# Performance work log

Measured on AMD Instinct MI355X. Metric: run time of the kernel, lower is better.

## Reference

```python
import jax, jax.numpy as jnp
import numpy as np
import math

N, E, D, H = 50000, 1600000, 128, 8
DH = D // H  # per-head dim
EPS = 1e-5   # batchnorm eps


def _attn(q_in, k_in, v_in, Wq, Wk, Wv, src, dst):
    # GAT-style edge attention: score = exp(clip(<K[src],Q[dst]>/sqrt(DH), -5, 5))
    Q = (q_in @ Wq.T).reshape(-1, H, DH)
    K = (k_in @ Wk.T).reshape(-1, H, DH)
    V = (v_in @ Wv.T).reshape(-1, H, DH)
    score = jnp.exp(jnp.clip((K[src] * Q[dst]).sum(-1) / math.sqrt(DH), -5.0, 5.0))  # [E,H]
    wV = jax.ops.segment_sum(V[src] * score[:, :, None], dst, num_segments=N)  # [N,H,DH]
    z = jax.ops.segment_sum(score, dst, num_segments=N)                         # [N,H]
    return (wV / z[:, :, None]).reshape(-1, D)


def _bn(x, gamma, beta):
    # BatchNorm1d in training mode: biased batch stats over nodes
    m = x.mean(0)
    v = x.var(0)
    return (x - m) / jnp.sqrt(v + EPS) * gamma + beta


def setup_inputs() -> dict:
    key = jax.random.key(0)
    ks = iter(jax.random.split(key, 48))

    def w(shape, scale=None):
        s = scale if scale is not None else 1.0 / math.sqrt(shape[-1])
        return jax.random.normal(next(ks), shape, jnp.float32) * s

    inp = dict(
        h=w((N, D), 1.0),
        sv=w((N, D), 1.0),
        src=jax.random.randint(next(ks), (E,), 0, N, jnp.int32),
        dst=jax.random.randint(next(ks), (E,), 0, N, jnp.int32),
    )
    for nm in ["Wq_sv", "Wk_sv", "Wv_sv", "Wq_cv", "Wk_cv", "Wv_cv",
               "Wq_sh", "Wk_sh", "Wv_sh"]:
        inp[nm] = w((D, D))
    inp.update(
        Wo=w((D, 2 * D)), bo=jnp.zeros((D,), jnp.float32),
        Wo_h=w((D, 2 * D)), bo_h=jnp.zeros((D,), jnp.float32),
        W1=w((2 * D, D)), b1=jnp.zeros((2 * D,), jnp.float32),
        W2=w((D, 2 * D)), b2=jnp.zeros((D,), jnp.float32),
        W1h=w((2 * D, D)), b1h=jnp.zeros((2 * D,), jnp.float32),
        W2h=w((D, 2 * D)), b2h=jnp.zeros((D,), jnp.float32),
        Wg1=w((D, D)), bg1=jnp.zeros((D,), jnp.float32),
        Wg2=w((D, D)), bg2=jnp.zeros((D,), jnp.float32),
        gbn1=jnp.ones((D,), jnp.float32), bbn1=jnp.zeros((D,), jnp.float32),
        gbn2=jnp.ones((D,), jnp.float32), bbn2=jnp.zeros((D,), jnp.float32),
        gbn1h=jnp.ones((D,), jnp.float32), bbn1h=jnp.zeros((D,), jnp.float32),
        gbn2h=jnp.ones((D,), jnp.float32), bbn2h=jnp.zeros((D,), jnp.float32),
    )
    return inp


def reference(h, sv, src, dst,
              Wq_sv, Wk_sv, Wv_sv, Wq_cv, Wk_cv, Wv_cv, Wq_sh, Wk_sh, Wv_sh,
              Wo, bo, Wo_h, bo_h,
              W1, b1, W2, b2, W1h, b1h, W2h, b2h,
              Wg1, bg1, Wg2, bg2,
              gbn1, bbn1, gbn2, bbn2, gbn1h, bbn1h, gbn2h, bbn2h):
    h_in1, sv_in1 = h, sv
    # --- h branch ---
    a_self = _attn(h, h, h, Wq_sv, Wk_sv, Wv_sv, src, dst)
    a_cross = _attn(h, sv, sv, Wq_cv, Wk_cv, Wv_cv, src, dst)
    hO = jnp.concatenate([a_self, a_cross], -1) @ Wo.T + bo
    h1 = _bn(h_in1 + hO, gbn1, bbn1)
    ffn = jax.nn.relu(h1 @ W1.T + b1) @ W2.T + b2
    h_out = _bn(h1 + ffn, gbn2, bbn2)
    # --- state-vector branch ---
    a_self_h = _attn(sv, sv, sv, Wq_sh, Wk_sh, Wv_sh, src, dst)
    # faithful to source: cross_attention_v weights reused here
    a_cross_h = _attn(sv, h_in1, h_in1, Wq_cv, Wk_cv, Wv_cv, src, dst)
    svO = jnp.concatenate([a_self_h, a_cross_h], -1) @ Wo_h.T + bo_h
    g1 = jax.nn.sigmoid(h_in1 @ Wg1.T + bg1)
    sv1 = _bn((1.0 - g1) * sv_in1 + g1 * svO, gbn1h, bbn1h)
    ffn_h = jax.nn.relu(sv1 @ W1h.T + b1h) @ W2h.T + b2h
    g2 = jax.nn.sigmoid(h_in1 @ Wg2.T + bg2)
    sv_out = _bn((1.0 - g2) * sv1 + g2 * ffn_h, gbn2h, bbn2h)
    return (h_out, sv_out)
```

## Files before the change

### kernel.cpp

```cpp
#include <hip/hip_runtime.h>

typedef _Float16 f16x8 __attribute__((ext_vector_type(8)));
typedef _Float16 f16x2 __attribute__((ext_vector_type(2)));
typedef __fp16 fp16x2_raw __attribute__((ext_vector_type(2)));
typedef float f32x4 __attribute__((ext_vector_type(4)));
typedef float f32x2 __attribute__((ext_vector_type(2)));
typedef unsigned int uint32;
typedef unsigned short ushort16;
typedef unsigned char uchar;

#define EPS_BN 1e-5f

__device__ __forceinline__ uint32 pk16(float a, float b){
  fp16x2_raw h = __builtin_amdgcn_cvt_pkrtz(a, b);
  return *(uint32*)&h;
}
__device__ __forceinline__ uchar f2fp8(float f){
  uint32 p = __builtin_amdgcn_cvt_pk_fp8_f32(f, f, 0, false);
  return (uchar)(p & 0xff);
}
__device__ __forceinline__ f32x2 fp8pair_lo(uint32 w){
  return __builtin_amdgcn_cvt_pk_f32_fp8(w, false);
}
__device__ __forceinline__ f32x2 fp8pair_hi(uint32 w){
  return __builtin_amdgcn_cvt_pk_f32_fp8(w, true);
}

struct WEnt { const float* s; const float* s2; ushort16* d; int KD, MD, nfrag; };
struct WConv { WEnt e[16]; };

__global__ __launch_bounds__(256) void conv_w_k(WConv a){
  WEnt t = a.e[blockIdx.y];
  int fid = blockIdx.x * 256 + threadIdx.x;
  if (fid >= t.nfrag) return;
  int lane = fid & 63, sm = fid >> 6;
  int MT = t.MD >> 4;
  int s = sm / MT, m = sm - s * MT;
  int row = m * 16 + (lane & 15);
  int col = s * 32 + (lane >> 4) * 8;
  const float* sp = t.s;
  if (t.s2 && row >= 128){ sp = t.s2; row -= 128; }
  const float* p = sp + (size_t)row * t.KD + col;
  uint4 o;
  o.x = pk16(p[0], p[1]); o.y = pk16(p[2], p[3]);
  o.z = pk16(p[4], p[5]); o.w = pk16(p[6], p[7]);
  *(uint4*)(t.d + (size_t)fid * 8) = o;
}

__global__ __launch_bounds__(256) void conv2_k(const float* __restrict__ a, const float* __restrict__ b,
                                               ushort16* __restrict__ da, ushort16* __restrict__ db, int n){
  const float* s = blockIdx.y ? b : a;
  ushort16* d = blockIdx.y ? db : da;
  int i = (blockIdx.x * 256 + threadIdx.x) * 4;
  if (i >= n) return;
  float4 v = *(const float4*)(s + i);
  uint2 p;
  p.x = pk16(v.x, v.y);
  p.y = pk16(v.z, v.w);
  *(uint2*)(d + i) = p;
}

__global__ void hist_k(const int* __restrict__ dst, int* __restrict__ cnt, int E){
  int i = blockIdx.x * blockDim.x + threadIdx.x;
  int stride = gridDim.x * blockDim.x;
  for (; i < E; i += stride) atomicAdd(&cnt[dst[i]], 1);
}

__global__ __launch_bounds__(256) void scan_part_k(const int* __restrict__ cnt, int* __restrict__ bsum, int N){
  int tid = threadIdx.x, lane = tid & 63, wv = tid >> 6;
  int base = blockIdx.x * 1024 + tid * 4;
  int ts = 0;
  #pragma unroll
  for (int j = 0; j < 4; j++) if (base + j < N) ts += cnt[base + j];
  #pragma unroll
  for (int d = 1; d < 64; d <<= 1) ts += __shfl_xor(ts, d);
  __shared__ int wt[4];
  if (lane == 0) wt[wv] = ts;
  __syncthreads();
  if (tid == 0) bsum[blockIdx.x] = wt[0] + wt[1] + wt[2] + wt[3];
}

__global__ __launch_bounds__(64) void scan_top_k(int* __restrict__ bsum, int nb){
  int tid = threadIdx.x;
  int v = (tid < nb) ? bsum[tid] : 0;
  int inc = v;
  #pragma unroll
  for (int d = 1; d < 64; d <<= 1){
    int t = __shfl_up(inc, d);
    if (tid >= d) inc += t;
  }
  if (tid < nb) bsum[tid] = inc - v;
}

__global__ __launch_bounds__(256) void scan_out_k(const int* __restrict__ cnt, const int* __restrict__ bsum,
                                                  int* __restrict__ row_off, int* __restrict__ cursor,
                                                  int* __restrict__ bcur,
                                                  int N, int E, int shift){
  int tid = threadIdx.x, lane = tid & 63, wv = tid >> 6;
  int base = blockIdx.x * 1024 + tid * 4;
  int c[4]; int ts = 0;
  #pragma unroll
  for (int j = 0; j < 4; j++){ c[j] = (base + j < N) ? cnt[base + j] : 0; ts += c[j]; }
  int inc = ts;
  #pragma unroll
  for (int d = 1; d < 64; d <<= 1){
    int t = __shfl_up(inc, d);
    if (lane >= d) inc += t;
  }
  int wexcl = inc - ts;
  __shared__ int wt[4];
  if (lane == 63) wt[wv] = inc;
  __syncthreads();
  int woff = 0;
  for (int w = 0; w < 4; w++) if (w < wv) woff += wt[w];
  int off = bsum[blockIdx.x] + woff + wexcl;
  int mask = (1 << shift) - 1;
  #pragma unroll
  for (int j = 0; j < 4; j++){
    int d = base + j;
    if (d < N){
      row_off[d] = off; cursor[d] = off;
      if ((d & mask) == 0) bcur[d >> shift] = off;
      off += c[j];
    }
  }
  if (blockIdx.x == 0 && tid == 0) row_off[N] = E;
}

#define BIN_TB 512
#define BIN_TILE 4096
__global__ __launch_bounds__(512) void bin_k(const int* __restrict__ src, const int* __restrict__ dst,
                                             int* __restrict__ bcur, uint2* __restrict__ ebuf,
                                             int E, int shift, int B){
  __shared__ int lhist[128];
  __shared__ int lstart[128];
  __shared__ int gbase[128];
  __shared__ uint2 lpair[BIN_TILE];
  int tid = threadIdx.x;
  int base = blockIdx.x * BIN_TILE;
  int cnt = E - base; if (cnt > BIN_TILE) cnt = BIN_TILE;
  if (tid < 128) lhist[tid] = 0;
  __syncthreads();
  int myb[8], myrank[8];
  uint2 myp[8];
  int nmine = 0;
  #pragma unroll
  for (int j = 0; j < 8; j++){
    int i = tid + j * BIN_TB;
    if (i < cnt){
      int s = src[base + i], d = dst[base + i];
      int b = d >> shift;
      myp[nmine] = make_uint2((uint32)s, (uint32)d);
      myb[nmine] = b;
      myrank[nmine] = atomicAdd(&lhist[b], 1);
      nmine++;
    }
  }
  __syncthreads();
  if (tid == 0){
    int run = 0;
    for (int b = 0; b < B; b++){ lstart[b] = run; run += lhist[b]; }
  }
  __syncthreads();
  if (tid < B) gbase[tid] = atomicAdd(&bcur[tid], lhist[tid]);
  for (int j = 0; j < nmine; j++){
    lpair[lstart[myb[j]] + myrank[j]] = myp[j];
  }
  __syncthreads();
  for (int i = tid; i < cnt; i += BIN_TB){
    uint2 p = lpair[i];
    int b = (int)(p.y >> shift);
    ebuf[gbase[b] + (i - lstart[b])] = p;
  }
}

#define BF_SPLIT 8
__global__ __launch_bounds__(256) void bfill_k(const uint2* __restrict__ ebuf, const int* __restrict__ row_off,
                                               int* __restrict__ cursor, int* __restrict__ esrc,
                                               int shift, int N){
  int b = blockIdx.x / BF_SPLIT, slice = blockIdx.x % BF_SPLIT;
  int d0 = b << shift;
  int d1 = (b + 1) << shift; if (d1 > N) d1 = N;
  if (d0 >= N) return;
  int e0 = row_off[d0], e1 = row_off[d1];
  for (int i = e0 + slice * 256 + (int)threadIdx.x; i < e1; i += 256 * BF_SPLIT){
    uint2 p = ebuf[i];
    int pos = atomicAdd(&cursor[p.y], 1);
    esrc[pos] = (int)p.x;
  }
}

struct QkvArgs {
  const ushort16* Xq[4];
  const ushort16* Xkv[4];
  const ushort16* Wq[4];
  const ushort16* Wk[4];
  const ushort16* Wv[4];
  ushort16* Qo[4];
};
__global__ __launch_bounds__(256) void gemm_qkv_k(
    QkvArgs A, uchar* __restrict__ KV8, int N)
{
  __shared__ _Float16 Qs[4][16 * 136];
  __shared__ uchar Ks[4][16 * 136];
  __shared__ uchar Vs[4][16 * 136];
  int slot = blockIdx.y;
  int toff = slot << 8;
  const ushort16* Xq = A.Xq[slot];
  const ushort16* Xkv = A.Xkv[slot];
  ushort16* Qo = A.Qo[slot];
  int lane = threadIdx.x & 63, wv = threadIdx.x >> 6;
  int l15 = lane & 15, kq = lane >> 4;
  int rowbase = (blockIdx.x * 4 + wv) * 16;
  int row = rowbase + l15;
  int rc = row < N ? row : N - 1;
  const f16x8* aq = (const f16x8*)(Xq + (size_t)rc * 128 + kq * 8);
  const f16x8* ak = (const f16x8*)(Xkv + (size_t)rc * 128 + kq * 8);
  f16x8 Aq[4], Ak[4];
  #pragma unroll
  for (int s = 0; s < 4; s++){ Aq[s] = aq[s * 4]; Ak[s] = ak[s * 4]; }
  const f16x8* Wqf = (const f16x8*)A.Wq[slot];
  const f16x8* Wkf = (const f16x8*)A.Wk[slot];
  const f16x8* Wvf = (const f16x8*)A.Wv[slot];
  f32x4 q[8], k[8], v[8];
  #pragma unroll
  for (int m = 0; m < 8; m++){ q[m] = (f32x4)(0.f); k[m] = (f32x4)(0.f); v[m] = (f32x4)(0.f); }
  #pragma unroll
  for (int s = 0; s < 4; s++){
    #pragma unroll
    for (int m = 0; m < 8; m++){
      int fi = (s * 8 + m) * 64 + lane;
      q[m] = __builtin_amdgcn_mfma_f32_16x16x32_f16(Aq[s], Wqf[fi], q[m], 0, 0, 0);
      k[m] = __builtin_amdgcn_mfma_f32_16x16x32_f16(Ak[s], Wkf[fi], k[m], 0, 0, 0);
      v[m] = __builtin_amdgcn_mfma_f32_16x16x32_f16(Ak[s], Wvf[fi], v[m], 0, 0, 0);
    }
  }
  #pragma unroll
  for (int m = 0; m < 8; m++){
    int col = m * 16 + l15;
    #pragma unroll
    for (int r = 0; r < 4; r++){
      int lrow = kq * 4 + r;
      Qs[wv][lrow * 136 + col] = (_Float16)q[m][r];
      Ks[wv][lrow * 136 + col] = f2fp8(k[m][r]);
      Vs[wv][lrow * 136 + col] = f2fp8(v[m][r]);
    }
  }
  #pragma unroll
  for (int p = 0; p < 4; p++){
    int lrow = p * 4 + (lane >> 4);
    int rr = rowbase + lrow;
    int col8 = l15 * 8;
    if (rr < N){
      uint4 qv = *(uint4*)&Qs[wv][lrow * 136 + col8];
      *(uint4*)(Qo + (size_t)rr * 128 + col8) = qv;
      uint2 kv = *(uint2*)&Ks[wv][lrow * 136 + col8];
      *(uint2*)(KV8 + (size_t)rr * 1024 + toff + col8) = kv;
      uint2 vv = *(uint2*)&Vs[wv][lrow * 136 + col8];
      *(uint2*)(KV8 + (size_t)rr * 1024 + toff + 128 + col8) = vv;
    }
  }
}

template<int KD, int MD, int EPI, int ABN, int ST, int GS>
__global__ __launch_bounds__(256) void gemm_k(
    const ushort16* __restrict__ X, const ushort16* __restrict__ W,
    const float* __restrict__ bias, const float* __restrict__ bias2,
    const ushort16* __restrict__ resb, const ushort16* __restrict__ gatep,
    const float* __restrict__ rstats, const float* __restrict__ rg, const float* __restrict__ rb,
    const float* __restrict__ astats, const float* __restrict__ ag, const float* __restrict__ ab,
    ushort16* __restrict__ outb, float* __restrict__ stats_out, int N, float invN)
{
  constexpr int KS = KD / 32;
  constexpr int MT = MD / 16;
  constexpr int LSTR = MD + 8;
  __shared__ _Float16 Os[4][16 * LSTR];
  int lane = threadIdx.x & 63, wv = threadIdx.x >> 6;
  int l15 = lane & 15, kq = lane >> 4;
  int rowbase = (blockIdx.x * 4 + wv) * 16;
  int row = rowbase + l15;
  int rc = row < N ? row : N - 1;
  const f16x8* ap = (const f16x8*)(X + (size_t)rc * KD + kq * 8);
  f16x8 a[KS];
  #pragma unroll
  for (int s = 0; s < KS; s++) a[s] = ap[s * 4];
  if constexpr (ABN){
    #pragma unroll
    for (int s = 0; s < KS; s++){
      #pragma unroll
      for (int j = 0; j < 8; j++){
        int c = s * 32 + kq * 8 + j;
        float mm = astats[c] * invN;
        float var = astats[128 + c] * invN - mm * mm;
        float rs = rsqrtf(var + EPS_BN);
        float scc = rs * ag[c];
        float shh = ab[c] - mm * scc;
        a[s][j] = (_Float16)((float)a[s][j] * scc + shh);
      }
    }
  }
  const f16x8* Wf = (const f16x8*)W;
  f32x4 acc[MT];
  #pragma unroll
  for (int m = 0; m < MT; m++) acc[m] = (f32x4)(0.f);
  #pragma unroll
  for (int s = 0; s < KS; s++){
    #pragma unroll
    for (int m = 0; m < MT; m++){
      acc[m] = __builtin_amdgcn_mfma_f32_16x16x32_f16(a[s], Wf[(s * MT + m) * 64 + lane], acc[m], 0, 0, 0);
    }
  }
  float ps[MT], ps2[MT];
  if constexpr (ST){
    #pragma unroll
    for (int m = 0; m < MT; m++){ ps[m] = 0.f; ps2[m] = 0.f; }
  }
  int r0 = rowbase + kq * 4;
  #pragma unroll
  for (int m = 0; m < MT; m++){
    int col = m * 16 + l15;
    float bv;
    if (bias2 && col >= 128) bv = bias2[col - 128];
    else bv = bias[col];
    float sc = 0.f, sh = 0.f;
    if constexpr (EPI == 5 || EPI == 6){
      float mm = rstats[col] * invN;
      float var = rstats[128 + col] * invN - mm * mm;
      float rs = rsqrtf(var + EPS_BN);
      sc = rs * rg[col]; sh = rb[col] - mm * sc;
    }
    #pragma unroll
    for (int r = 0; r < 4; r++){
      int rr = r0 + r;
      float v;
      {
        int rrc = rr < N ? rr : N - 1;
        v = acc[m][r] + bv;
        if constexpr (EPI == 1) v = fmaxf(v, 0.f);
        if constexpr (EPI == 2) v = 1.f / (1.f + __expf(-v));
        if constexpr (EPI == 3){
          union { ushort16 u; _Float16 h; } cv; cv.u = resb[(size_t)rrc * 128 + col];
          v += (float)cv.h;
        }
        if constexpr (EPI == 5){
          union { ushort16 u; _Float16 h; } cv; cv.u = resb[(size_t)rrc * 128 + col];
          v += (float)cv.h * sc + sh;
        }
        if constexpr (EPI == 4 || EPI == 6){
          union { ushort16 u; _Float16 h; } gv; gv.u = gatep[(size_t)rrc * GS + col];
          union { ushort16 u; _Float16 h; } cv; cv.u = resb[(size_t)rrc * 128 + col];
          float g = (float)gv.h;
          float rv = (float)cv.h;
          if constexpr (EPI == 6) rv = rv * sc + sh;
          v = (1.f - g) * rv + g * v;
        }
      }
      Os[wv][(kq * 4 + r) * LSTR + col] = (_Float16)v;
      if constexpr (ST){
        if (rr < N){ ps[m] += v; ps2[m] += v * v; }
      }
    }
  }
  if constexpr (MD == 128){
    #pragma unroll
    for (int p = 0; p < 4; p++){
      int lrow = p * 4 + (lane >> 4);
      int rr = rowbase + lrow;
      int col8 = l15 * 8;
      if (rr < N){
        uint4 ov = *(uint4*)&Os[wv][lrow * LSTR + col8];
        *(uint4*)(outb + (size_t)rr * MD + col8) = ov;
      }
    }
  } else {
    #pragma unroll
    for (int p = 0; p < 8; p++){
      int lrow = p * 2 + (lane >> 5);
      int rr = rowbase + lrow;
      int col8 = (lane & 31) * 8;
      if (rr < N){
        uint4 ov = *(uint4*)&Os[wv][lrow * LSTR + col8];
        *(uint4*)(outb + (size_t)rr * MD + col8) = ov;
      }
    }
  }
  if constexpr (ST){
    __shared__ float sst[4][128];
    __shared__ float sst2[4][128];
    #pragma unroll
    for (int m = 0; m < MT; m++){
      float s = ps[m], s2 = ps2[m];
      s  += __shfl_xor(s, 16);  s  += __shfl_xor(s, 32);
      s2 += __shfl_xor(s2, 16); s2 += __shfl_xor(s2, 32);
      if (lane < 16){ sst[wv][m * 16 + l15] = s; sst2[wv][m * 16 + l15] = s2; }
    }
    __syncthreads();
    int tid = threadIdx.x;
    if (tid < 128){
      atomicAdd(&stats_out[tid], sst[0][tid] + sst[1][tid] + sst[2][tid] + sst[3][tid]);
    } else {
      int c = tid - 128;
      atomicAdd(&stats_out[tid], sst2[0][c] + sst2[1][c] + sst2[2][c] + sst2[3][c]);
    }
  }
}

__global__ __launch_bounds__(256) void attn4_k(
    const ushort16* __restrict__ Qa, const ushort16* __restrict__ Qb,
    const ushort16* __restrict__ Qc, const ushort16* __restrict__ Qd,
    const uchar* __restrict__ KV,
    const int* __restrict__ row_off, const int* __restrict__ esrc,
    ushort16* __restrict__ cat_h, ushort16* __restrict__ cat_sv, int N)
{
  int wv = threadIdx.x >> 6, lane = threadIdx.x & 63;
  int n = blockIdx.x * 4 + wv;
  if (n >= N) return;
  int g = lane >> 4, j = lane & 15;
  uint32 j8 = (uint32)j * 8u;
  const float QS = 0.25f * 1.44269504088896f;
  const float CL = 7.21347520444482f;
  const ushort16* Qp[4] = {Qa, Qb, Qc, Qd};
  f32x2 q[4][4];
  #pragma unroll
  for (int t = 0; t < 4; t++){
    uint4 u = *(const uint4*)(Qp[t] + (size_t)n * 128 + j8);
    f16x2 h0 = *(f16x2*)&u.x, h1 = *(f16x2*)&u.y;
    f16x2 h2 = *(f16x2*)&u.z, h3 = *(f16x2*)&u.w;
    q[t][0].x = (float)h0.x * QS; q[t][0].y = (float)h0.y * QS;
    q[t][1].x = (float)h1.x * QS; q[t][1].y = (float)h1.y * QS;
    q[t][2].x = (float)h2.x * QS; q[t][2].y = (float)h2.y * QS;
    q[t][3].x = (float)h3.x * QS; q[t][3].y = (float)h3.y * QS;
  }
  int e0 = row_off[n], e1 = row_off[n + 1];
  int itmax = (e1 - e0 + 3) >> 2;
  f32x2 ac[4][4];
  #pragma unroll
  for (int t = 0; t < 4; t++){
    #pragma unroll
    for (int r = 0; r < 4; r++) ac[t][r] = (f32x2)(0.f);
  }
  float z[4] = {0.f, 0.f, 0.f, 0.f};
  int e = e0 + g;
  int s = (e < e1) ? esrc[e] : -1;
  uint32 off = ((uint32)(s < 0 ? 0 : s) << 10) + j8;
  uint2 kc[4], vc[4];
  #pragma unroll
  for (int t = 0; t < 4; t++){
    kc[t] = *(const uint2*)(KV + off + t * 256);
    vc[t] = *(const uint2*)(KV + off + t * 256 + 128);
  }
  for (int it = 0; it < itmax; ++it){
    int e2 = e + 4;
    int s2 = (e2 < e1) ? esrc[e2] : -1;
    uint32 off2 = ((uint32)(s2 < 0 ? 0 : s2) << 10) + j8;
    uint2 kn[4], vn[4];
    #pragma unroll
    for (int t = 0; t < 4; t++){
      kn[t] = *(const uint2*)(KV + off2 + t * 256);
      vn[t] = *(const uint2*)(KV + off2 + t * 256 + 128);
    }
    if (s >= 0){
      #pragma unroll
      for (int t = 0; t < 4; t++){
        f32x2 k0 = fp8pair_lo(kc[t].x), k1 = fp8pair_hi(kc[t].x);
        f32x2 k2 = fp8pair_lo(kc[t].y), k3 = fp8pair_hi(kc[t].y);
        f32x2 dd = k0 * q[t][0] + k1 * q[t][1] + k2 * q[t][2] + k3 * q[t][3];
        float d = dd.x + dd.y;
        d += __shfl_xor(d, 1);
        float sc = __builtin_amdgcn_exp2f(__builtin_amdgcn_fmed3f(d, -CL, CL));
        f32x2 v0 = fp8pair_lo(vc[t].x), v1 = fp8pair_hi(vc[t].x);
        f32x2 v2 = fp8pair_lo(vc[t].y), v3 = fp8pair_hi(vc[t].y);
        f32x2 sv; sv.x = sc; sv.y = sc;
        ac[t][0] += sv * v0; ac[t][1] += sv * v1;
        ac[t][2] += sv * v2; ac[t][3] += sv * v3;
        z[t] += sc;
      }
    }
    e = e2; s = s2; off = off2;
    #pragma unroll
    for (int t = 0; t < 4; t++){ kc[t] = kn[t]; vc[t] = vn[t]; }
  }
  #pragma unroll
  for (int t = 0; t < 4; t++){
    #pragma unroll
    for (int r = 0; r < 4; r++){
      ac[t][r].x += __shfl_xor(ac[t][r].x, 16);
      ac[t][r].y += __shfl_xor(ac[t][r].y, 16);
      ac[t][r].x += __shfl_xor(ac[t][r].x, 32);
      ac[t][r].y += __shfl_xor(ac[t][r].y, 32);
    }
    z[t] += __shfl_xor(z[t], 16);
    z[t] += __shfl_xor(z[t], 32);
  }
  if (g == 0){
    size_t base = (size_t)n * 256 + j8;
    #pragma unroll
    for (int t = 0; t < 4; t++){
      float rz = __builtin_amdgcn_rcpf(z[t]);
      uint4 o;
      o.x = pk16(ac[t][0].x * rz, ac[t][0].y * rz);
      o.y = pk16(ac[t][1].x * rz, ac[t][1].y * rz);
      o.z = pk16(ac[t][2].x * rz, ac[t][2].y * rz);
      o.w = pk16(ac[t][3].x * rz, ac[t][3].y * rz);
      ushort16* dp = (t < 2) ? cat_h : cat_sv;
      *(uint4*)(dp + base + (t & 1) * 128) = o;
    }
  }
}

__global__ __launch_bounds__(256) void bn_apply_k(
    const ushort16* __restrict__ x, const float* __restrict__ stats,
    const float* __restrict__ gamma, const float* __restrict__ beta,
    float* __restrict__ outf, int total4, float invN)
{
  int i = blockIdx.x * 256 + threadIdx.x;
  if (i >= total4) return;
  uint2 xp = *(const uint2*)(x + (size_t)i * 4);
  f16x2 x01 = *(f16x2*)&xp.x, x23 = *(f16x2*)&xp.y;
  float xv[4] = {(float)x01.x, (float)x01.y, (float)x23.x, (float)x23.y};
  int c0 = (i * 4) & 127;
  float o[4];
  #pragma unroll
  for (int j = 0; j < 4; j++){
    int c = c0 + j;
    float m = stats[c] * invN;
    float var = stats[128 + c] * invN - m * m;
    float rstd = rsqrtf(var + EPS_BN);
    o[j] = (xv[j] - m) * rstd * gamma[c] + beta[c];
  }
  *(float4*)(outf + (size_t)i * 4) = make_float4(o[0], o[1], o[2], o[3]);
}

extern "C" void kernel_launch(void* const* d_in, const int* in_sizes, int n_in,
                              void* d_out, int out_size, void* d_ws, size_t ws_size,
                              hipStream_t stream) {
  const float* h   = (const float*)d_in[0];
  const float* sv  = (const float*)d_in[1];
  const int* src   = (const int*)d_in[2];
  const int* dst   = (const int*)d_in[3];
  const int N = in_sizes[0] / 128;
  const int E = in_sizes[2];

  char* wsb = (char*)d_ws;
  size_t o = 0;
  auto take = [&](size_t bytes)->size_t{
    size_t r = o;
    o = (o + bytes + 255) & ~(size_t)255;
    return r;
  };
  size_t big = (size_t)E * 8;
  if (big < (size_t)N * 1024) big = (size_t)N * 1024;
  size_t cnt_off    = take((size_t)N * 4);
  size_t stats_off  = take(4 * 256 * 4);
  size_t rowoff_off = take((size_t)(N + 1) * 4);
  size_t cursor_off = take((size_t)N * 4);
  size_t bsum_off   = take(256 * 4);
  size_t bcur_off   = take(128 * 4);
  size_t esrc_off   = take((size_t)E * 4);
  size_t big_off    = take(big);
  size_t wpool_off  = take((size_t)376832 * 2);
  size_t hf_off     = take((size_t)N * 128 * 2);
  size_t svf_off    = take((size_t)N * 128 * 2);
  size_t cath_off   = take((size_t)N * 256 * 2);
  size_t catsv_off  = take((size_t)N * 256 * 2);
  size_t Q1_off     = take((size_t)N * 128 * 2);
  size_t Q2_off     = take((size_t)N * 128 * 2);
  size_t X1_off     = take((size_t)N * 128 * 2);
  size_t X2_off     = take((size_t)N * 128 * 2);

  int*    cnt     = (int*)(wsb + cnt_off);
  float*  stats   = (float*)(wsb + stats_off);
  int*    row_off = (int*)(wsb + rowoff_off);
  int*    cursor  = (int*)(wsb + cursor_off);
  int*    bsum    = (int*)(wsb + bsum_off);
  int*    bcur    = (int*)(wsb + bcur_off);
  int*    esrc    = (int*)(wsb + esrc_off);
  uint2*  ebuf    = (uint2*)(wsb + big_off);
  uchar*  KVall   = (uchar*)(wsb + big_off);
  ushort16* Gb16  = (ushort16*)(wsb + big_off);
  ushort16* wpool = (ushort16*)(wsb + wpool_off);
  ushort16* h_f   = (ushort16*)(wsb + hf_off);
  ushort16* sv_f  = (ushort16*)(wsb + svf_off);
  ushort16* cat_h = (ushort16*)(wsb + cath_off);
  ushort16* cat_sv= (ushort16*)(wsb + catsv_off);
  ushort16* Q1    = (ushort16*)(wsb + Q1_off);
  ushort16* Q2    = (ushort16*)(wsb + Q2_off);
  ushort16* Xb1   = (ushort16*)(wsb + X1_off);
  ushort16* Xb2   = (ushort16*)(wsb + X2_off);
  ushort16* Q3 = Xb1;
  ushort16* Q4 = Xb2;

  ushort16* Wq_sv = wpool + 0 * 16384;
  ushort16* Wk_sv = wpool + 1 * 16384;
  ushort16* Wv_sv = wpool + 2 * 16384;
  ushort16* Wq_cv = wpool + 3 * 16384;
  ushort16* Wk_cv = wpool + 4 * 16384;
  ushort16* Wv_cv = wpool + 5 * 16384;
  ushort16* Wq_sh = wpool + 6 * 16384;
  ushort16* Wk_sh = wpool + 7 * 16384;
  ushort16* Wv_sh = wpool + 8 * 16384;
  ushort16* Wgb   = wpool + 147456;
  ushort16* Wob   = wpool + 180224;
  ushort16* Wohb  = wpool + 212992;
  ushort16* W1b   = wpool + 245760;
  ushort16* W2b   = wpool + 278528;
  ushort16* W1hb  = wpool + 311296;
  ushort16* W2hb  = wpool + 344064;

  const float* bo   = (const float*)d_in[14];
  const float* bo_h = (const float*)d_in[16];
  const float* b1   = (const float*)d_in[18];
  const float* b2   = (const float*)d_in[20];
  const float* b1h  = (const float*)d_in[22];
  const float* b2h  = (const float*)d_in[24];
  const float* bg1  = (const float*)d_in[26];
  const float* bg2  = (const float*)d_in[28];
  const float* gbn1  = (const float*)d_in[29];
  const float* bbn1  = (const float*)d_in[30];
  const float* gbn2  = (const float*)d_in[31];
  const float* bbn2  = (const float*)d_in[32];
  const float* gbn1h = (const float*)d_in[33];
  const float* bbn1h = (const float*)d_in[34];
  const float* gbn2h = (const float*)d_in[35];
  const float* bbn2h = (const float*)d_in[36];

  float* out_h  = (float*)d_out;
  float* out_sv = out_h + (size_t)N * 128;

  (void)hipMemsetAsync(wsb, 0, stats_off + 4 * 256 * 4, stream);

  WConv wc;
  {
    auto set = [&](int i, int din, int din2, size_t dstoff, int KD, int MD){
      wc.e[i].s  = (const float*)d_in[din];
      wc.e[i].s2 = (din2 >= 0) ? (const float*)d_in[din2] : nullptr;
      wc.e[i].d  = wpool + dstoff;
      wc.e[i].KD = KD; wc.e[i].MD = MD;
      wc.e[i].nfrag = KD * MD / 8;
    };
    for (int i = 0; i < 9; i++) set(i, 4 + i, -1, (size_t)i * 16384, 128, 128);
    set(9,  25, 27, 147456, 128, 256);
    set(10, 13, -1, 180224, 256, 128);
    set(11, 15, -1, 212992, 256, 128);
    set(12, 17, -1, 245760, 128, 256);
    set(13, 19, -1, 278528, 256, 128);
    set(14, 21, -1, 311296, 128, 256);
    set(15, 23, -1, 344064, 256, 128);
  }
  conv_w_k<<<dim3(16, 16), 256, 0, stream>>>(wc);

  int nelem = N * 128;
  conv2_k<<<dim3((nelem / 4 + 255) / 256, 2), 256, 0, stream>>>(h, sv, h_f, sv_f, nelem);

  int shift = 9;
  while ((((N - 1) >> shift) + 1) > 128) shift++;
  const int B = ((N - 1) >> shift) + 1;

  const int NB = (N + 1023) / 1024;
  hist_k<<<2048, 256, 0, stream>>>(dst, cnt, E);
  scan_part_k<<<NB, 256, 0, stream>>>(cnt, bsum, N);
  scan_top_k<<<1, 64, 0, stream>>>(bsum, NB);
  scan_out_k<<<NB, 256, 0, stream>>>(cnt, bsum, row_off, cursor, bcur, N, E, shift);
  bin_k<<<(E + BIN_TILE - 1) / BIN_TILE, BIN_TB, 0, stream>>>(src, dst, bcur, ebuf, E, shift, B);
  bfill_k<<<B * BF_SPLIT, 256, 0, stream>>>(ebuf, row_off, cursor, esrc, shift, N);

  const int GB = (N + 63) / 64;
  const int AB = (N + 3) / 4;
  const int T4 = nelem / 4;
  const int APB = (T4 + 255) / 256;
  const float invN = 1.f / (float)N;

  QkvArgs qa;
  qa.Xq[0] = h_f;  qa.Xkv[0] = h_f;  qa.Wq[0] = Wq_sv; qa.Wk[0] = Wk_sv; qa.Wv[0] = Wv_sv; qa.Qo[0] = Q1;
  qa.Xq[1] = h_f;  qa.Xkv[1] = sv_f; qa.Wq[1] = Wq_cv; qa.Wk[1] = Wk_cv; qa.Wv[1] = Wv_cv; qa.Qo[1] = Q2;
  qa.Xq[2] = sv_f; qa.Xkv[2] = sv_f; qa.Wq[2] = Wq_sh; qa.Wk[2] = Wk_sh; qa.Wv[2] = Wv_sh; qa.Qo[2] = Q3;
  qa.Xq[3] = sv_f; qa.Xkv[3] = h_f;  qa.Wq[3] = Wq_cv; qa.Wk[3] = Wk_cv; qa.Wv[3] = Wv_cv; qa.Qo[3] = Q4;
  gemm_qkv_k<<<dim3(GB, 4), 256, 0, stream>>>(qa, KVall, N);
  attn4_k<<<AB, 256, 0, stream>>>(Q1, Q2, Q3, Q4, KVall, row_off, esrc, cat_h, cat_sv, N);

  gemm_k<256,128,3,0,1,256><<<GB, 256, 0, stream>>>(cat_h, Wob, bo, nullptr, h_f, nullptr,
      nullptr, nullptr, nullptr, nullptr, nullptr, nullptr, Xb1, stats, N, invN);
  gemm_k<128,256,1,1,0,256><<<GB, 256, 0, stream>>>(Xb1, W1b, b1, nullptr, nullptr, nullptr,
      nullptr, nullptr, nullptr, stats, gbn1, bbn1, cat_h, nullptr, N, invN);
  gemm_k<256,128,5,0,1,256><<<GB, 256, 0, stream>>>(cat_h, W2b, b2, nullptr, Xb1, nullptr,
      stats, gbn1, bbn1, nullptr, nullptr, nullptr, Xb2, stats + 256, N, invN);
  bn_apply_k<<<APB, 256, 0, stream>>>(Xb2, stats + 256, gbn2, bbn2, out_h, T4, invN);

  gemm_k<128,256,2,0,0,256><<<GB, 256, 0, stream>>>(h_f, Wgb, bg1, bg2, nullptr, nullptr,
      nullptr, nullptr, nullptr, nullptr, nullptr, nullptr, Gb16, nullptr, N, invN);
  gemm_k<256,128,4,0,1,256><<<GB, 256, 0, stream>>>(cat_sv, Wohb, bo_h, nullptr, sv_f, Gb16,
      nullptr, nullptr, nullptr, nullptr, nullptr, nullptr, Xb1, stats + 512, N, invN);
  gemm_k<128,256,1,1,0,256><<<GB, 256, 0, stream>>>(Xb1, W1hb, b1h, nullptr, nullptr, nullptr,
      nullptr, nullptr, nullptr, stats + 512, gbn1h, bbn1h, cat_sv, nullptr, N, invN);
  gemm_k<256,128,6,0,1,256><<<GB, 256, 0, stream>>>(cat_sv, W2hb, b2h, nullptr, Xb1, Gb16 + 128,
      stats + 512, gbn1h, bbn1h, nullptr, nullptr, nullptr, Xb2, stats + 768, N, invN);
  bn_apply_k<<<APB, 256, 0, stream>>>(Xb2, stats + 768, gbn2h, bbn2h, out_sv, T4, invN);
}
```

Baseline: 856.6 us.

## Batch paired branch GEMMs and BN into shared launches, merge prep kernels

Merges the f16 conversion and destination histogram into one launch. Folds the top-level scan into scan_out_k, where each block sums the preceding block totals itself. Runs the h-branch and sv-branch output-projection, FFN1, FFN2 and final BN as paired kernels with a grid y dimension of 2, and moves the gate GEMM ahead of attention into a dedicated buffer. This cuts the launch count and doubles per-launch parallelism for the mid-sized GEMMs, at the cost of an extra workspace buffer and reusing Q1/Q2 as intermediates.

```diff
diff --git a/kernel.cpp b/kernel.cpp
--- a/kernel.cpp
+++ b/kernel.cpp
@@ -47,23 +47,24 @@
   *(uint4*)(t.d + (size_t)fid * 8) = o;
 }
 
-__global__ __launch_bounds__(256) void conv2_k(const float* __restrict__ a, const float* __restrict__ b,
-                                               ushort16* __restrict__ da, ushort16* __restrict__ db, int n){
-  const float* s = blockIdx.y ? b : a;
-  ushort16* d = blockIdx.y ? db : da;
-  int i = (blockIdx.x * 256 + threadIdx.x) * 4;
-  if (i >= n) return;
-  float4 v = *(const float4*)(s + i);
-  uint2 p;
-  p.x = pk16(v.x, v.y);
-  p.y = pk16(v.z, v.w);
-  *(uint2*)(d + i) = p;
-}
-
-__global__ void hist_k(const int* __restrict__ dst, int* __restrict__ cnt, int E){
-  int i = blockIdx.x * blockDim.x + threadIdx.x;
-  int stride = gridDim.x * blockDim.x;
-  for (; i < E; i += stride) atomicAdd(&cnt[dst[i]], 1);
+__global__ __launch_bounds__(256) void conv2h_k(const float* __restrict__ a, const float* __restrict__ b,
+                                                ushort16* __restrict__ da, ushort16* __restrict__ db, int n,
+                                                const int* __restrict__ dst, int* __restrict__ cnt, int E){
+  if (blockIdx.y < 2){
+    const float* s = blockIdx.y ? b : a;
+    ushort16* d = blockIdx.y ? db : da;
+    int i = (blockIdx.x * 256 + threadIdx.x) * 4;
+    if (i >= n) return;
+    float4 v = *(const float4*)(s + i);
+    uint2 p;
+    p.x = pk16(v.x, v.y);
+    p.y = pk16(v.z, v.w);
+    *(uint2*)(d + i) = p;
+  } else {
+    int i = blockIdx.x * 256 + threadIdx.x;
+    int stride = gridDim.x * 256;
+    for (; i < E; i += stride) atomicAdd(&cnt[dst[i]], 1);
+  }
 }
 
 __global__ __launch_bounds__(256) void scan_part_k(const int* __restrict__ cnt, int* __restrict__ bsum, int N){
@@ -80,23 +81,15 @@
   if (tid == 0) bsum[blockIdx.x] = wt[0] + wt[1] + wt[2] + wt[3];
 }
 
-__global__ __launch_bounds__(64) void scan_top_k(int* __restrict__ bsum, int nb){
-  int tid = threadIdx.x;
-  int v = (tid < nb) ? bsum[tid] : 0;
-  int inc = v;
-  #pragma unroll
-  for (int d = 1; d < 64; d <<= 1){
-    int t = __shfl_up(inc, d);
-    if (tid >= d) inc += t;
-  }
-  if (tid < nb) bsum[tid] = inc - v;
-}
-
 __global__ __launch_bounds__(256) void scan_out_k(const int* __restrict__ cnt, const int* __restrict__ bsum,
                                                   int* __restrict__ row_off, int* __restrict__ cursor,
                                                   int* __restrict__ bcur,
                                                   int N, int E, int shift){
   int tid = threadIdx.x, lane = tid & 63, wv = tid >> 6;
+  int bp = 0;
+  for (int i = lane; i < (int)blockIdx.x; i += 64) bp += bsum[i];
+  #pragma unroll
+  for (int d = 1; d < 64; d <<= 1) bp += __shfl_xor(bp, d);
   int base = blockIdx.x * 1024 + tid * 4;
   int c[4]; int ts = 0;
   #pragma unroll
@@ -113,7 +106,7 @@
   __syncthreads();
   int woff = 0;
   for (int w = 0; w < 4; w++) if (w < wv) woff += wt[w];
-  int off = bsum[blockIdx.x] + woff + wexcl;
+  int off = bp + woff + wexcl;
   int mask = (1 << shift) - 1;
   #pragma unroll
   for (int j = 0; j < 4; j++){
@@ -263,19 +256,20 @@
 }
 
 template<int KD, int MD, int EPI, int ABN, int ST, int GS>
-__global__ __launch_bounds__(256) void gemm_k(
+__device__ __forceinline__ void gemm_body(
     const ushort16* __restrict__ X, const ushort16* __restrict__ W,
     const float* __restrict__ bias, const float* __restrict__ bias2,
     const ushort16* __restrict__ resb, const ushort16* __restrict__ gatep,
     const float* __restrict__ rstats, const float* __restrict__ rg, const float* __restrict__ rb,
     const float* __restrict__ astats, const float* __restrict__ ag, const float* __restrict__ ab,
-    ushort16* __restrict__ outb, float* __restrict__ stats_out, int N, float invN)
+    ushort16* __restrict__ outb, float* __restrict__ stats_out, int N, float invN,
+    _Float16* OsBase, float* sstB, float* sst2B)
 {
   constexpr int KS = KD / 32;
   constexpr int MT = MD / 16;
   constexpr int LSTR = MD + 8;
-  __shared__ _Float16 Os[4][16 * LSTR];
   int lane = threadIdx.x & 63, wv = threadIdx.x >> 6;
+  _Float16* OsW = OsBase + wv * 16 * LSTR;
   int l15 = lane & 15, kq = lane >> 4;
   int rowbase = (blockIdx.x * 4 + wv) * 16;
   int row = rowbase + l15;
@@ -355,7 +349,7 @@
           v = (1.f - g) * rv + g * v;
         }
       }
-      Os[wv][(kq * 4 + r) * LSTR + col] = (_Float16)v;
+      OsW[(kq * 4 + r) * LSTR + col] = (_Float16)v;
       if constexpr (ST){
         if (rr < N){ ps[m] += v; ps2[m] += v * v; }
       }
@@ -368,7 +362,7 @@
       int rr = rowbase + lrow;
       int col8 = l15 * 8;
       if (rr < N){
-        uint4 ov = *(uint4*)&Os[wv][lrow * LSTR + col8];
+        uint4 ov = *(uint4*)&OsW[lrow * LSTR + col8];
         *(uint4*)(outb + (size_t)rr * MD + col8) = ov;
       }
     }
@@ -379,29 +373,69 @@
       int rr = rowbase + lrow;
       int col8 = (lane & 31) * 8;
       if (rr < N){
-        uint4 ov = *(uint4*)&Os[wv][lrow * LSTR + col8];
+        uint4 ov = *(uint4*)&OsW[lrow * LSTR + col8];
         *(uint4*)(outb + (size_t)rr * MD + col8) = ov;
       }
     }
   }
   if constexpr (ST){
-    __shared__ float sst[4][128];
-    __shared__ float sst2[4][128];
     #pragma unroll
     for (int m = 0; m < MT; m++){
       float s = ps[m], s2 = ps2[m];
       s  += __shfl_xor(s, 16);  s  += __shfl_xor(s, 32);
       s2 += __shfl_xor(s2, 16); s2 += __shfl_xor(s2, 32);
-      if (lane < 16){ sst[wv][m * 16 + l15] = s; sst2[wv][m * 16 + l15] = s2; }
+      if (lane < 16){ sstB[wv * 128 + m * 16 + l15] = s; sst2B[wv * 128 + m * 16 + l15] = s2; }
     }
     __syncthreads();
     int tid = threadIdx.x;
     if (tid < 128){
-      atomicAdd(&stats_out[tid], sst[0][tid] + sst[1][tid] + sst[2][tid] + sst[3][tid]);
+      atomicAdd(&stats_out[tid], sstB[tid] + sstB[128 + tid] + sstB[256 + tid] + sstB[384 + tid]);
     } else {
       int c = tid - 128;
-      atomicAdd(&stats_out[tid], sst2[0][c] + sst2[1][c] + sst2[2][c] + sst2[3][c]);
-    }
+      atomicAdd(&stats_out[tid], sst2B[c] + sst2B[128 + c] + sst2B[256 + c] + sst2B[384 + c]);
+    }
+  }
+}
+
+template<int KD, int MD, int EPI, int ABN, int ST, int GS>
+__global__ __launch_bounds__(256) void gemm_k(
+    const ushort16* __restrict__ X, const ushort16* __restrict__ W,
+    const float* __restrict__ bias, const float* __restrict__ bias2,
+    const ushort16* __restrict__ resb, const ushort16* __restrict__ gatep,
+    const float* __restrict__ rstats, const float* __restrict__ rg, const float* __restrict__ rb,
+    const float* __restrict__ astats, const float* __restrict__ ag, const float* __restrict__ ab,
+    ushort16* __restrict__ outb, float* __restrict__ stats_out, int N, float invN)
+{
+  __shared__ _Float16 Os[4 * 16 * (MD + 8)];
+  __shared__ float sst[512];
+  __shared__ float sst2[512];
+  gemm_body<KD, MD, EPI, ABN, ST, GS>(X, W, bias, bias2, resb, gatep, rstats, rg, rb,
+                                      astats, ag, ab, outb, stats_out, N, invN, Os, sst, sst2);
+}
+
+struct GPairArgs {
+  const ushort16* X[2]; const ushort16* W[2];
+  const float* bias[2];
+  const ushort16* resb[2]; const ushort16* gatep[2];
+  const float* rstats[2]; const float* rg[2]; const float* rb[2];
+  const float* astats[2]; const float* ag[2]; const float* ab[2];
+  ushort16* outb[2]; float* stats_out[2];
+};
+template<int KD, int MD, int EPI0, int EPI1, int ABN, int ST, int GS>
+__global__ __launch_bounds__(256) void gemm_pair_k(GPairArgs A, int N, float invN)
+{
+  __shared__ _Float16 Os[4 * 16 * (MD + 8)];
+  __shared__ float sst[512];
+  __shared__ float sst2[512];
+  int y = blockIdx.y;
+  if (y == 0){
+    gemm_body<KD, MD, EPI0, ABN, ST, GS>(A.X[0], A.W[0], A.bias[0], nullptr, A.resb[0], A.gatep[0],
+        A.rstats[0], A.rg[0], A.rb[0], A.astats[0], A.ag[0], A.ab[0],
+        A.outb[0], A.stats_out[0], N, invN, Os, sst, sst2);
+  } else {
+    gemm_body<KD, MD, EPI1, ABN, ST, GS>(A.X[1], A.W[1], A.bias[1], nullptr, A.resb[1], A.gatep[1],
+        A.rstats[1], A.rg[1], A.rb[1], A.astats[1], A.ag[1], A.ab[1],
+        A.outb[1], A.stats_out[1], N, invN, Os, sst, sst2);
   }
 }
 
@@ -508,13 +542,20 @@
   }
 }
 
-__global__ __launch_bounds__(256) void bn_apply_k(
-    const ushort16* __restrict__ x, const float* __restrict__ stats,
-    const float* __restrict__ gamma, const float* __restrict__ beta,
-    float* __restrict__ outf, int total4, float invN)
+struct Bn2Args {
+  const ushort16* x[2]; const float* stats[2];
+  const float* g[2]; const float* b[2]; float* out[2];
+};
+__global__ __launch_bounds__(256) void bn2_k(Bn2Args A, int total4, float invN)
 {
+  int y = blockIdx.y;
   int i = blockIdx.x * 256 + threadIdx.x;
   if (i >= total4) return;
+  const ushort16* x = A.x[y];
+  const float* stats = A.stats[y];
+  const float* gamma = A.g[y];
+  const float* beta = A.b[y];
+  float* outf = A.out[y];
   uint2 xp = *(const uint2*)(x + (size_t)i * 4);
   f16x2 x01 = *(f16x2*)&xp.x, x23 = *(f16x2*)&xp.y;
   float xv[4] = {(float)x01.x, (float)x01.y, (float)x23.x, (float)x23.y};
@@ -567,6 +608,7 @@
   size_t Q2_off     = take((size_t)N * 128 * 2);
   size_t X1_off     = take((size_t)N * 128 * 2);
   size_t X2_off     = take((size_t)N * 128 * 2);
+  size_t G_off      = take((size_t)N * 256 * 2);
 
   int*    cnt     = (int*)(wsb + cnt_off);
   float*  stats   = (float*)(wsb + stats_off);
@@ -577,7 +619,6 @@
   int*    esrc    = (int*)(wsb + esrc_off);
   uint2*  ebuf    = (uint2*)(wsb + big_off);
   uchar*  KVall   = (uchar*)(wsb + big_off);
-  ushort16* Gb16  = (ushort16*)(wsb + big_off);
   ushort16* wpool = (ushort16*)(wsb + wpool_off);
   ushort16* h_f   = (ushort16*)(wsb + hf_off);
   ushort16* sv_f  = (ushort16*)(wsb + svf_off);
@@ -587,6 +628,7 @@
   ushort16* Q2    = (ushort16*)(wsb + Q2_off);
   ushort16* Xb1   = (ushort16*)(wsb + X1_off);
   ushort16* Xb2   = (ushort16*)(wsb + X2_off);
+  ushort16* Gbuf  = (ushort16*)(wsb + G_off);
   ushort16* Q3 = Xb1;
   ushort16* Q4 = Xb2;
 
@@ -650,16 +692,15 @@
   conv_w_k<<<dim3(16, 16), 256, 0, stream>>>(wc);
 
   int nelem = N * 128;
-  conv2_k<<<dim3((nelem / 4 + 255) / 256, 2), 256, 0, stream>>>(h, sv, h_f, sv_f, nelem);
+  int CVB = (nelem / 4 + 255) / 256;
+  conv2h_k<<<dim3(CVB, 3), 256, 0, stream>>>(h, sv, h_f, sv_f, nelem, dst, cnt, E);
 
   int shift = 9;
   while ((((N - 1) >> shift) + 1) > 128) shift++;
   const int B = ((N - 1) >> shift) + 1;
 
   const int NB = (N + 1023) / 1024;
-  hist_k<<<2048, 256, 0, stream>>>(dst, cnt, E);
   scan_part_k<<<NB, 256, 0, stream>>>(cnt, bsum, N);
-  scan_top_k<<<1, 64, 0, stream>>>(bsum, NB);
   scan_out_k<<<NB, 256, 0, stream>>>(cnt, bsum, row_off, cursor, bcur, N, E, shift);
   bin_k<<<(E + BIN_TILE - 1) / BIN_TILE, BIN_TB, 0, stream>>>(src, dst, bcur, ebuf, E, shift, B);
   bfill_k<<<B * BF_SPLIT, 256, 0, stream>>>(ebuf, row_off, cursor, esrc, shift, N);
@@ -669,6 +710,9 @@
   const int T4 = nelem / 4;
   const int APB = (T4 + 255) / 256;
   const float invN = 1.f / (float)N;
+
+  gemm_k<128,256,2,0,0,256><<<GB, 256, 0, stream>>>(h_f, Wgb, bg1, bg2, nullptr, nullptr,
+      nullptr, nullptr, nullptr, nullptr, nullptr, nullptr, Gbuf, nullptr, N, invN);
 
   QkvArgs qa;
   qa.Xq[0] = h_f;  qa.Xkv[0] = h_f;  qa.Wq[0] = Wq_sv; qa.Wk[0] = Wk_sv; qa.Wv[0] = Wv_sv; qa.Qo[0] = Q1;
@@ -678,21 +722,36 @@
   gemm_qkv_k<<<dim3(GB, 4), 256, 0, stream>>>(qa, KVall, N);
   attn4_k<<<AB, 256, 0, stream>>>(Q1, Q2, Q3, Q4, KVall, row_off, esrc, cat_h, cat_sv, N);
 
-  gemm_k<256,128,3,0,1,256><<<GB, 256, 0, stream>>>(cat_h, Wob, bo, nullptr, h_f, nullptr,
-      nullptr, nullptr, nullptr, nullptr, nullptr, nullptr, Xb1, stats, N, invN);
-  gemm_k<128,256,1,1,0,256><<<GB, 256, 0, stream>>>(Xb1, W1b, b1, nullptr, nullptr, nullptr,
-      nullptr, nullptr, nullptr, stats, gbn1, bbn1, cat_h, nullptr, N, invN);
-  gemm_k<256,128,5,0,1,256><<<GB, 256, 0, stream>>>(cat_h, W2b, b2, nullptr, Xb1, nullptr,
-      stats, gbn1, bbn1, nullptr, nullptr, nullptr, Xb2, stats + 256, N, invN);
-  bn_apply_k<<<APB, 256, 0, stream>>>(Xb2, stats + 256, gbn2, bbn2, out_h, T4, invN);
-
-  gemm_k<128,256,2,0,0,256><<<GB, 256, 0, stream>>>(h_f, Wgb, bg1, bg2, nullptr, nullptr,
-      nullptr, nullptr, nullptr, nullptr, nullptr, nullptr, Gb16, nullptr, N, invN);
-  gemm_k<256,128,4,0,1,256><<<GB, 256, 0, stream>>>(cat_sv, Wohb, bo_h, nullptr, sv_f, Gb16,
-      nullptr, nullptr, nullptr, nullptr, nullptr, nullptr, Xb1, stats + 512, N, invN);
-  gemm_k<128,256,1,1,0,256><<<GB, 256, 0, stream>>>(Xb1, W1hb, b1h, nullptr, nullptr, nullptr,
-      nullptr, nullptr, nullptr, stats + 512, gbn1h, bbn1h, cat_sv, nullptr, N, invN);
-  gemm_k<256,128,6,0,1,256><<<GB, 256, 0, stream>>>(cat_sv, W2hb, b2h, nullptr, Xb1, Gb16 + 128,
-      stats + 512, gbn1h, bbn1h, nullptr, nullptr, nullptr, Xb2, stats + 768, N, invN);
-  bn_apply_k<<<APB, 256, 0, stream>>>(Xb2, stats + 768, gbn2h, bbn2h, out_sv, T4, invN);
-}
+  {
+    GPairArgs A = {};
+    A.X[0] = cat_h;  A.W[0] = Wob;  A.bias[0] = bo;   A.resb[0] = h_f;  A.gatep[0] = nullptr;
+    A.outb[0] = Xb1; A.stats_out[0] = stats;
+    A.X[1] = cat_sv; A.W[1] = Wohb; A.bias[1] = bo_h; A.resb[1] = sv_f; A.gatep[1] = Gbuf;
+    A.outb[1] = Q1;  A.stats_out[1] = stats + 512;
+    gemm_pair_k<256,128,3,4,0,1,256><<<dim3(GB, 2), 256, 0, stream>>>(A, N, invN);
+  }
+  {
+    GPairArgs A = {};
+    A.X[0] = Xb1; A.W[0] = W1b;  A.bias[0] = b1;
+    A.astats[0] = stats;       A.ag[0] = gbn1;  A.ab[0] = bbn1;  A.outb[0] = cat_h;
+    A.X[1] = Q1;  A.W[1] = W1hb; A.bias[1] = b1h;
+    A.astats[1] = stats + 512; A.ag[1] = gbn1h; A.ab[1] = bbn1h; A.outb[1] = cat_sv;
+    gemm_pair_k<128,256,1,1,1,0,256><<<dim3(GB, 2), 256, 0, stream>>>(A, N, invN);
+  }
+  {
+    GPairArgs A = {};
+    A.X[0] = cat_h;  A.W[0] = W2b;  A.bias[0] = b2;  A.resb[0] = Xb1;
+    A.rstats[0] = stats;       A.rg[0] = gbn1;  A.rb[0] = bbn1;
+    A.outb[0] = Xb2; A.stats_out[0] = stats + 256;
+    A.X[1] = cat_sv; A.W[1] = W2hb; A.bias[1] = b2h; A.resb[1] = Q1;  A.gatep[1] = Gbuf + 128;
+    A.rstats[1] = stats + 512; A.rg[1] = gbn1h; A.rb[1] = bbn1h;
+    A.outb[1] = Q2;  A.stats_out[1] = stats + 768;
+    gemm_pair_k<256,128,5,6,0,1,256><<<dim3(GB, 2), 256, 0, stream>>>(A, N, invN);
+  }
+  {
+    Bn2Args A;
+    A.x[0] = Xb2; A.stats[0] = stats + 256; A.g[0] = gbn2;  A.b[0] = bbn2;  A.out[0] = out_h;
+    A.x[1] = Q2;  A.stats[1] = stats + 768; A.g[1] = gbn2h; A.b[1] = bbn2h; A.out[1] = out_sv;
+    bn2_k<<<dim3(APB, 2), 256, 0, stream>>>(A, T4, invN);
+  }
+}
```

Result: faster. 818.8 us (-4.4%).
